# Performance work log

Hardware: AMD Instinct MI355X
Metric: run time of the kernel (lower is better)

Reference implementation:

```python
import jax, jax.numpy as jnp
from jax import lax
import numpy as np

B, T, DD, DS, H = 512, 365, 5, 27, 256


def setup_inputs() -> dict:
    key = jax.random.key(0)
    ks = jax.random.split(key, 12)
    s = lambda fan_in: 1.0 / np.sqrt(fan_in)
    return {
        "x_dynamic": jax.random.normal(ks[0], (B, T, DD), jnp.float32),
        "x_static": jax.random.normal(ks[1], (B, DS), jnp.float32),
        "Wi": jax.random.normal(ks[2], (DS, H), jnp.float32) * s(DS),
        "bi": jax.random.normal(ks[3], (H,), jnp.float32) * s(DS),
        "Wf": jax.random.normal(ks[4], (DS, H), jnp.float32) * s(DS),
        "bf": jax.random.normal(ks[5], (H,), jnp.float32) * s(DS),
        "Wg": jax.random.normal(ks[6], (DD + H, H), jnp.float32) * s(DD + H),
        "bg": jax.random.normal(ks[7], (H,), jnp.float32) * s(DD + H),
        "Wo": jax.random.normal(ks[8], (DD + H, H), jnp.float32) * s(DD + H),
        "bo": jax.random.normal(ks[9], (H,), jnp.float32) * s(DD + H),
        "Wh": jax.random.normal(ks[10], (H, 1), jnp.float32) * s(H),
        "bh": jax.random.normal(ks[11], (1,), jnp.float32) * s(H),
    }


def reference(x_dynamic, x_static, Wi, bi, Wf, bf, Wg, bg, Wo, bo, Wh, bh):
    # Entity-aware gates depend only on static input -> compute once, reuse every step.
    i = jax.nn.sigmoid(x_static @ Wi + bi)  # [B, H]
    f = jax.nn.sigmoid(x_static @ Wf + bf)  # [B, H]

    bsz = x_dynamic.shape[0]
    hid = Wi.shape[1]
    h0 = jnp.zeros((bsz, hid), x_dynamic.dtype)
    c0 = jnp.zeros((bsz, hid), x_dynamic.dtype)

    def step(carry, x_t):
        h, c = carry
        comb = jnp.concatenate([x_t, h], axis=1)          # [B, DD+H]
        g = jnp.tanh(comb @ Wg + bg)
        o = jax.nn.sigmoid(comb @ Wo + bo)
        c_next = f * c + i * g
        h_next = o * jnp.tanh(c_next)
        return (h_next, c_next), None

    xs = jnp.swapaxes(x_dynamic, 0, 1)  # [T, B, DD]
    (h, _), _ = lax.scan(step, (h0, c0), xs)

    # Dropout is identity in eval mode.
    return h @ Wh + bh  # [B, 1]
```

## Files before the change

kernel.cpp:

```cpp
#include <hip/hip_runtime.h>

#define B_   512
#define T_   365
#define DD_  5
#define DS_  27
#define H_   256
#define ROWS 2
#define NBLK (B_ / ROWS)
#define NW   8
#define NTHR (NW * 64)
#define HP   288

typedef _Float16 half8_t __attribute__((ext_vector_type(8)));
typedef float    f32x4   __attribute__((ext_vector_type(4)));

#define LOG2E_ 1.4426950408889634f

__device__ __forceinline__ float sigmoid_f(float x) {
    return __builtin_amdgcn_rcpf(1.0f + __builtin_amdgcn_exp2f(-x * LOG2E_));
}
__device__ __forceinline__ float tanh_f(float x) {
    return 1.0f - 2.0f * __builtin_amdgcn_rcpf(1.0f + __builtin_amdgcn_exp2f(2.0f * LOG2E_ * x));
}

__global__ __launch_bounds__(NTHR, 2)
void ealstm_kernel(const float* __restrict__ xdyn,
                   const float* __restrict__ xstat,
                   const float* __restrict__ Wi, const float* __restrict__ bi,
                   const float* __restrict__ Wf, const float* __restrict__ bf_,
                   const float* __restrict__ Wg, const float* __restrict__ bg,
                   const float* __restrict__ Wo, const float* __restrict__ bo,
                   const float* __restrict__ Wh, const float* __restrict__ bh,
                   float* __restrict__ out)
{
    const int tid = threadIdx.x;
    const int l   = tid & 63;
    const int w   = tid >> 6;
    const int b0  = blockIdx.x * ROWS;

    __shared__ __align__(16) _Float16 hbuf[2][2][HP];
    __shared__ __align__(16) float xsh[ROWS][T_][8];
    __shared__ float red[2][NW];

    {
        _Float16* hz = &hbuf[0][0][0];
        for (int i = tid; i < 2 * 2 * HP; i += NTHR) hz[i] = (_Float16)0.0f;
    }
    for (int i = tid; i < ROWS * T_ * DD_; i += NTHR) {
        int r   = i / (T_ * DD_);
        int rem = i - r * (T_ * DD_);
        int tt  = rem / DD_;
        int d   = rem - tt * DD_;
        xsh[r][tt][d] = xdyn[(size_t)(b0 + r) * (T_ * DD_) + rem];
    }

    const int colW = w * 32;
    const int lg   = l >> 4;
    const int lm   = l & 15;
    half8_t Bf[2][2][8];
    {
#pragma unroll
        for (int m = 0; m < 2; ++m) {
            const float* Ws = (m == 0) ? Wg : Wo;
#pragma unroll
            for (int tt = 0; tt < 2; ++tt) {
#pragma unroll
                for (int ks = 0; ks < 8; ++ks) {
                    int col = colW + tt * 16 + lm;
                    int k   = ks * 32 + 8 * lg;
                    const float* p = Ws + (size_t)(DD_ + k) * H_ + col;
                    half8_t v;
#pragma unroll
                    for (int i = 0; i < 8; ++i) v[i] = (_Float16)p[(size_t)i * H_];
                    Bf[m][tt][ks] = v;
                }
            }
        }
    }

    const int r_l = (l >> 4) & 1;
    const int c_l = colW + (l >> 5) * 16 + lm;

    float Wgx[DD_], Wox[DD_];
#pragma unroll
    for (int d = 0; d < DD_; ++d) {
        Wgx[d] = Wg[d * H_ + c_l];
        Wox[d] = Wo[d * H_ + c_l];
    }
    const float bgv = bg[c_l], bov = bo[c_l];

    float iG, fG, cst = 0.0f;
    {
        float ai = bi[c_l], af = bf_[c_l];
        for (int d = 0; d < DS_; ++d) {
            float xv = xstat[(b0 + r_l) * DS_ + d];
            ai += xv * Wi[d * H_ + c_l];
            af += xv * Wf[d * H_ + c_l];
        }
        iG = sigmoid_f(ai);
        fG = sigmoid_f(af);
    }

    half8_t Af[8];
    {
        half8_t z;
#pragma unroll
        for (int i = 0; i < 8; ++i) z[i] = (_Float16)0.0f;
#pragma unroll
        for (int ks = 0; ks < 8; ++ks) Af[ks] = z;
    }
    const bool areal = ((lm & 3) == 0);
    const int  arow  = (lm >> 2) & 1;
    const bool low   = (l < 32);

    __syncthreads();

    float xg, xo;
    {
        const float4 xv = *(const float4*)&xsh[r_l][0][0];
        const float  x4 = xsh[r_l][0][4];
        xg = bgv + xv.x*Wgx[0] + xv.y*Wgx[1] + xv.z*Wgx[2] + xv.w*Wgx[3] + x4*Wgx[4];
        xo = bov + xv.x*Wox[0] + xv.y*Wox[1] + xv.z*Wox[2] + xv.w*Wox[3] + x4*Wox[4];
    }

#pragma unroll 2
    for (int t = 0; t < T_; ++t) {
        const int cur = t & 1;
        const int nxt = cur ^ 1;

        if (areal) {
#pragma unroll
            for (int ks = 0; ks < 8; ++ks)
                Af[ks] = *(const half8_t*)&hbuf[cur][arow][ks * 32 + 8 * lg];
        }

        const int tn = (t + 1 < T_) ? t + 1 : t;
        const float4 xvn = *(const float4*)&xsh[r_l][tn][0];
        const float  x4n = xsh[r_l][tn][4];

        f32x4 accG0 = {0.f,0.f,0.f,0.f}, accG1 = {0.f,0.f,0.f,0.f};
        f32x4 accO0 = {0.f,0.f,0.f,0.f}, accO1 = {0.f,0.f,0.f,0.f};
        __builtin_amdgcn_s_setprio(1);
#pragma unroll
        for (int ks = 0; ks < 8; ++ks) {
            accG0 = __builtin_amdgcn_mfma_f32_16x16x32_f16(Af[ks], Bf[0][0][ks], accG0, 0, 0, 0);
            accG1 = __builtin_amdgcn_mfma_f32_16x16x32_f16(Af[ks], Bf[0][1][ks], accG1, 0, 0, 0);
            accO0 = __builtin_amdgcn_mfma_f32_16x16x32_f16(Af[ks], Bf[1][0][ks], accO0, 0, 0, 0);
            accO1 = __builtin_amdgcn_mfma_f32_16x16x32_f16(Af[ks], Bf[1][1][ks], accO1, 0, 0, 0);
        }
        __builtin_amdgcn_s_setprio(0);

        float pg = (low ? accG0[0] : accG1[0]) + xg;
        float po = (low ? accO0[0] : accO1[0]) + xo;

        float g = tanh_f(pg);
        float o = sigmoid_f(po);
        cst = fG * cst + iG * g;
        float hv = o * tanh_f(cst);
        hbuf[nxt][r_l][c_l] = (_Float16)hv;

        xg = bgv + xvn.x*Wgx[0] + xvn.y*Wgx[1] + xvn.z*Wgx[2] + xvn.w*Wgx[3] + x4n*Wgx[4];
        xo = bov + xvn.x*Wox[0] + xvn.y*Wox[1] + xvn.z*Wox[2] + xvn.w*Wox[3] + x4n*Wox[4];

        __syncthreads();
    }

    const int fin  = T_ & 1;
    const int oc   = tid & 255;
    const int orow = tid >> 8;
    float v = (float)hbuf[fin][orow][oc] * Wh[oc];
#pragma unroll
    for (int off = 32; off > 0; off >>= 1)
        v += __shfl_down(v, off);
    if (l == 0) red[orow][w & 3] = v;
    __syncthreads();
    if (tid < ROWS) {
        out[b0 + tid] = red[tid][0] + red[tid][1] + red[tid][2] + red[tid][3] + bh[0];
    }
}

extern "C" void kernel_launch(void* const* d_in, const int* in_sizes, int n_in,
                              void* d_out, int out_size, void* d_ws, size_t ws_size,
                              hipStream_t stream) {
    (void)in_sizes; (void)n_in; (void)out_size; (void)d_ws; (void)ws_size;
    const float* xdyn  = (const float*)d_in[0];
    const float* xstat = (const float*)d_in[1];
    const float* Wi    = (const float*)d_in[2];
    const float* bi    = (const float*)d_in[3];
    const float* Wf    = (const float*)d_in[4];
    const float* bf    = (const float*)d_in[5];
    const float* Wg    = (const float*)d_in[6];
    const float* bg    = (const float*)d_in[7];
    const float* Wo    = (const float*)d_in[8];
    const float* bo    = (const float*)d_in[9];
    const float* Wh    = (const float*)d_in[10];
    const float* bh    = (const float*)d_in[11];
    float* out = (float*)d_out;

    hipLaunchKernelGGL(ealstm_kernel, dim3(NBLK), dim3(NTHR), 0, stream,
                       xdyn, xstat, Wi, bi, Wf, bf, Wg, bg, Wo, bo, Wh, bh, out);
}
```

Before: 263.3 us.

## Split hidden columns across 16 waves with one 16-column tile each

Doubles the waves per block from 8 to 16, so each wave owns 16 hidden columns instead of 32. Each timestep then runs 16 MFMAs per wave instead of 32, and the B-fragment registers per wave are halved. The aim is a shorter serial critical path per step and lower register pressure. In exchange, the per-step block barrier must now sync twice as many waves, half the lanes in each wave do redundant gate math without writing, and per-block register demand may limit occupancy.

```diff
diff --git a/kernel.cpp b/kernel.cpp
--- a/kernel.cpp
+++ b/kernel.cpp
@@ -7,7 +7,7 @@
 #define H_   256
 #define ROWS 2
 #define NBLK (B_ / ROWS)
-#define NW   8
+#define NW   16
 #define NTHR (NW * 64)
 #define HP   288
 
@@ -23,7 +23,7 @@
     return 1.0f - 2.0f * __builtin_amdgcn_rcpf(1.0f + __builtin_amdgcn_exp2f(2.0f * LOG2E_ * x));
 }
 
-__global__ __launch_bounds__(NTHR, 2)
+__global__ __launch_bounds__(NTHR, 4)
 void ealstm_kernel(const float* __restrict__ xdyn,
                    const float* __restrict__ xstat,
                    const float* __restrict__ Wi, const float* __restrict__ bi,
@@ -40,7 +40,7 @@
 
     __shared__ __align__(16) _Float16 hbuf[2][2][HP];
     __shared__ __align__(16) float xsh[ROWS][T_][8];
-    __shared__ float red[2][NW];
+    __shared__ float red[2][8];
 
     {
         _Float16* hz = &hbuf[0][0][0];
@@ -54,32 +54,29 @@
         xsh[r][tt][d] = xdyn[(size_t)(b0 + r) * (T_ * DD_) + rem];
     }
 
-    const int colW = w * 32;
+    const int colW = w * 16;
     const int lg   = l >> 4;
     const int lm   = l & 15;
-    half8_t Bf[2][2][8];
+    half8_t Bf[2][8];
     {
 #pragma unroll
         for (int m = 0; m < 2; ++m) {
             const float* Ws = (m == 0) ? Wg : Wo;
 #pragma unroll
-            for (int tt = 0; tt < 2; ++tt) {
+            for (int ks = 0; ks < 8; ++ks) {
+                int col = colW + lm;
+                int k   = ks * 32 + 8 * lg;
+                const float* p = Ws + (size_t)(DD_ + k) * H_ + col;
+                half8_t v;
 #pragma unroll
-                for (int ks = 0; ks < 8; ++ks) {
-                    int col = colW + tt * 16 + lm;
-                    int k   = ks * 32 + 8 * lg;
-                    const float* p = Ws + (size_t)(DD_ + k) * H_ + col;
-                    half8_t v;
-#pragma unroll
-                    for (int i = 0; i < 8; ++i) v[i] = (_Float16)p[(size_t)i * H_];
-                    Bf[m][tt][ks] = v;
-                }
+                for (int i = 0; i < 8; ++i) v[i] = (_Float16)p[(size_t)i * H_];
+                Bf[m][ks] = v;
             }
         }
     }
 
     const int r_l = (l >> 4) & 1;
-    const int c_l = colW + (l >> 5) * 16 + lm;
+    const int c_l = colW + lm;
 
     float Wgx[DD_], Wox[DD_];
 #pragma unroll
@@ -111,7 +108,7 @@
     }
     const bool areal = ((lm & 3) == 0);
     const int  arow  = (lm >> 2) & 1;
-    const bool low   = (l < 32);
+    const bool wr    = (l < 32);
 
     __syncthreads();
 
@@ -138,26 +135,23 @@
         const float4 xvn = *(const float4*)&xsh[r_l][tn][0];
         const float  x4n = xsh[r_l][tn][4];
 
-        f32x4 accG0 = {0.f,0.f,0.f,0.f}, accG1 = {0.f,0.f,0.f,0.f};
-        f32x4 accO0 = {0.f,0.f,0.f,0.f}, accO1 = {0.f,0.f,0.f,0.f};
+        f32x4 accG = {0.f,0.f,0.f,0.f}, accO = {0.f,0.f,0.f,0.f};
         __builtin_amdgcn_s_setprio(1);
 #pragma unroll
         for (int ks = 0; ks < 8; ++ks) {
-            accG0 = __builtin_amdgcn_mfma_f32_16x16x32_f16(Af[ks], Bf[0][0][ks], accG0, 0, 0, 0);
-            accG1 = __builtin_amdgcn_mfma_f32_16x16x32_f16(Af[ks], Bf[0][1][ks], accG1, 0, 0, 0);
-            accO0 = __builtin_amdgcn_mfma_f32_16x16x32_f16(Af[ks], Bf[1][0][ks], accO0, 0, 0, 0);
-            accO1 = __builtin_amdgcn_mfma_f32_16x16x32_f16(Af[ks], Bf[1][1][ks], accO1, 0, 0, 0);
+            accG = __builtin_amdgcn_mfma_f32_16x16x32_f16(Af[ks], Bf[0][ks], accG, 0, 0, 0);
+            accO = __builtin_amdgcn_mfma_f32_16x16x32_f16(Af[ks], Bf[1][ks], accO, 0, 0, 0);
         }
         __builtin_amdgcn_s_setprio(0);
 
-        float pg = (low ? accG0[0] : accG1[0]) + xg;
-        float po = (low ? accO0[0] : accO1[0]) + xo;
+        float pg = accG[0] + xg;
+        float po = accO[0] + xo;
 
         float g = tanh_f(pg);
         float o = sigmoid_f(po);
         cst = fG * cst + iG * g;
         float hv = o * tanh_f(cst);
-        hbuf[nxt][r_l][c_l] = (_Float16)hv;
+        if (wr) hbuf[nxt][r_l][c_l] = (_Float16)hv;
 
         xg = bgv + xvn.x*Wgx[0] + xvn.y*Wgx[1] + xvn.z*Wgx[2] + xvn.w*Wgx[3] + x4n*Wgx[4];
         xo = bov + xvn.x*Wox[0] + xvn.y*Wox[1] + xvn.z*Wox[2] + xvn.w*Wox[3] + x4n*Wox[4];
@@ -165,14 +159,16 @@
         __syncthreads();
     }
 
-    const int fin  = T_ & 1;
-    const int oc   = tid & 255;
-    const int orow = tid >> 8;
-    float v = (float)hbuf[fin][orow][oc] * Wh[oc];
+    const int fin = T_ & 1;
+    if (tid < 512) {
+        const int oc   = tid & 255;
+        const int orow = tid >> 8;
+        float v = (float)hbuf[fin][orow][oc] * Wh[oc];
 #pragma unroll
-    for (int off = 32; off > 0; off >>= 1)
-        v += __shfl_down(v, off);
-    if (l == 0) red[orow][w & 3] = v;
+        for (int off = 32; off > 0; off >>= 1)
+            v += __shfl_down(v, off);
+        if (l == 0) red[orow][w & 3] = v;
+    }
     __syncthreads();
     if (tid < ROWS) {
         out[b0 + tid] = red[tid][0] + red[tid][1] + red[tid][2] + red[tid][3] + bh[0];
```

Measured after the change: 472.1 us. 1.79x slower.
